# Kernel optimization log

Hardware: AMD Instinct MI355X
Metric: run time of the kernel (lower is better)

Reference implementation:

```python
import jax, jax.numpy as jnp
import numpy as np

B, S, D, H = 2, 4096, 512, 8
HD = D // H

def setup_inputs() -> dict:
    key = jax.random.key(0)
    ks = jax.random.split(key, 11)
    s = 1.0 / np.sqrt(D)
    return {
        "x": jax.random.normal(ks[0], (B, S, D), jnp.float32),
        "y": jax.random.normal(ks[1], (B, S, D), jnp.float32),
        "z": jax.random.normal(ks[2], (B, S, D), jnp.float32),
        "Wq": jax.random.normal(ks[3], (D, D), jnp.float32) * s,
        "bq": jnp.zeros((D,), jnp.float32),
        "Wk": jax.random.normal(ks[4], (D, D), jnp.float32) * s,
        "bk": jnp.zeros((D,), jnp.float32),
        "Wv": jax.random.normal(ks[5], (D, D), jnp.float32) * s,
        "bv": jnp.zeros((D,), jnp.float32),
        "Wp": jax.random.normal(ks[6], (D, D), jnp.float32) * s,
        "bp": jnp.zeros((D,), jnp.float32),
    }

def reference(x, y, z, Wq, bq, Wk, bk, Wv, bv, Wp, bp):
    # q/k/v projections, split heads: [B,S,D] -> [B,H,S,HD]
    def heads(t):
        return t.reshape(B, -1, H, HD).transpose(0, 2, 1, 3)
    q = heads(x @ Wq + bq)
    k = heads(y @ Wk + bk)
    v = heads(z @ Wv + bv)
    att = jnp.einsum('bhqd,bhkd->bhqk', q, k) / np.sqrt(HD).astype(np.float32)
    att = jax.nn.softmax(att, axis=-1)  # dropout is identity in eval mode
    out = jnp.einsum('bhqk,bhkd->bhqd', att, v)
    out = out.transpose(0, 2, 1, 3).reshape(B, -1, D)
    return out @ Wp + bp
```

## Files before the change

kernel.cpp:

```cpp
#include <hip/hip_runtime.h>
#include <math.h>

#define B_ 2
#define S_ 4096
#define D_ 512
#define H_ 8
#define HD_ 64
#define NROW_ (B_ * S_)
#define NELEM_ ((size_t)NROW_ * D_)
#define WELEM_ ((size_t)D_ * D_)
#define QSC 0.18033688f

typedef _Float16 half8 __attribute__((ext_vector_type(8)));
typedef _Float16 half4v __attribute__((ext_vector_type(4)));
typedef __fp16 fp16x2 __attribute__((ext_vector_type(2)));
typedef float floatx4 __attribute__((ext_vector_type(4)));

__device__ __forceinline__ half8 cvt_half8(float4 a, float4 b) {
  fp16x2 l0 = __builtin_amdgcn_cvt_pkrtz(a.x, a.y);
  fp16x2 l1 = __builtin_amdgcn_cvt_pkrtz(a.z, a.w);
  fp16x2 l2 = __builtin_amdgcn_cvt_pkrtz(b.x, b.y);
  fp16x2 l3 = __builtin_amdgcn_cvt_pkrtz(b.z, b.w);
  half8 h;
  h[0] = l0[0]; h[1] = l0[1]; h[2] = l1[0]; h[3] = l1[1];
  h[4] = l2[0]; h[5] = l2[1]; h[6] = l3[0]; h[7] = l3[1];
  return h;
}

__device__ __forceinline__ void async_lds16(const _Float16* g,
                                            _Float16* l) {
  __builtin_amdgcn_global_load_lds(
      (const __attribute__((address_space(1))) void*)g,
      (__attribute__((address_space(3))) void*)l, 16, 0, 0);
}

struct WPtrs { const float *W0, *W1, *W2, *W3; };

__global__ void wT4_kernel(WPtrs p, _Float16* __restrict__ WTbase) {
  __shared__ float tl[32][33];
  const int z = blockIdx.z;
  const float* W = z == 0 ? p.W0 : z == 1 ? p.W1 : z == 2 ? p.W2 : p.W3;
  const float scale = z == 0 ? QSC : 1.0f;
  _Float16* Wt = WTbase + (size_t)z * WELEM_;
  const int t = threadIdx.x;
  const int k0 = blockIdx.y * 32, n0 = blockIdx.x * 32;
  const int r = t >> 3, c0 = (t & 7) * 4;
  const float4 v = *(const float4*)&W[(size_t)(k0 + r) * D_ + n0 + c0];
  tl[r][c0 + 0] = v.x; tl[r][c0 + 1] = v.y;
  tl[r][c0 + 2] = v.z; tl[r][c0 + 3] = v.w;
  __syncthreads();
  half4v hv;
#pragma unroll
  for (int j = 0; j < 4; ++j) hv[j] = (_Float16)(tl[c0 + j][r] * scale);
  *(half4v*)&Wt[(size_t)(n0 + r) * D_ + k0 + c0] = hv;
}

__global__ void vT_kernel(const _Float16* __restrict__ Vh,
                          _Float16* __restrict__ VhT) {
  __shared__ alignas(16) _Float16 T[64][72];
  const int t = threadIdx.x;
  const int s0 = blockIdx.x * 64;
  const int h = blockIdx.y, b = blockIdx.z;
  const int srow = t >> 3, soff = (t & 7) * 8;
#pragma unroll
  for (int i = 0; i < 2; ++i)
    *(half8*)&T[srow + 32 * i][soff] = *(const half8*)
        &Vh[(size_t)(b * S_ + s0 + srow + 32 * i) * D_ + h * HD_ + soff];
  __syncthreads();
  const size_t obase = (size_t)(b * H_ + h) * HD_ * S_;
#pragma unroll
  for (int i = 0; i < 2; ++i) {
    half8 o;
#pragma unroll
    for (int j = 0; j < 8; ++j) o[j] = T[soff + j][srow + 32 * i];
    *(half8*)&VhT[obase + (size_t)(srow + 32 * i) * S_ + s0 + soff] = o;
  }
}

template <bool AF16, bool OUT16, int BM>
__device__ __forceinline__ void gemm_body(
    const void* __restrict__ Av, const _Float16* __restrict__ Bt,
    const float* __restrict__ bias, void* __restrict__ Cout, float bscale,
    int bx, int by, int tid) {
  constexpr int MT = BM / 32;
  __shared__ alignas(16) _Float16 As[BM][72];
  __shared__ alignas(16) _Float16 Bs[128][72];

  const int w = tid >> 6, lane = tid & 63;
  const int m = lane & 15, quad = lane >> 4;
  const int row0 = by * BM, col0 = bx * 128;
  const int wr = (w >> 1) * (BM / 2), wc = (w & 1) * 64;
  const int srow = tid >> 3, soff = (tid & 7) * 8;

  const _Float16* A16 = (const _Float16*)Av;
  const float* A32 = (const float*)Av;

  floatx4 acc[MT][4];
#pragma unroll
  for (int i = 0; i < MT; ++i)
#pragma unroll
    for (int j = 0; j < 4; ++j) acc[i][j] = floatx4{0.f, 0.f, 0.f, 0.f};

  half8 pa16[MT];
  float4 pa32[MT][2];
  half8 pb[4];
#pragma unroll
  for (int i = 0; i < MT; ++i) {
    const size_t ar = (size_t)(row0 + srow + 32 * i) * D_ + soff;
    if (AF16) pa16[i] = *(const half8*)&A16[ar];
    else { pa32[i][0] = *(const float4*)&A32[ar];
           pa32[i][1] = *(const float4*)&A32[ar + 4]; }
  }
#pragma unroll
  for (int i = 0; i < 4; ++i)
    pb[i] = *(const half8*)&Bt[(size_t)(col0 + srow + 32 * i) * D_ + soff];

  for (int kt = 0; kt < D_ / 64; ++kt) {
    if (kt) __syncthreads();
#pragma unroll
    for (int i = 0; i < MT; ++i)
      *(half8*)&As[srow + 32 * i][soff] =
          AF16 ? pa16[i] : cvt_half8(pa32[i][0], pa32[i][1]);
#pragma unroll
    for (int i = 0; i < 4; ++i) *(half8*)&Bs[srow + 32 * i][soff] = pb[i];
    __syncthreads();
    if (kt < D_ / 64 - 1) {
      const int kc = (kt + 1) * 64 + soff;
#pragma unroll
      for (int i = 0; i < MT; ++i) {
        const size_t ar = (size_t)(row0 + srow + 32 * i) * D_ + kc;
        if (AF16) pa16[i] = *(const half8*)&A16[ar];
        else { pa32[i][0] = *(const float4*)&A32[ar];
               pa32[i][1] = *(const float4*)&A32[ar + 4]; }
      }
#pragma unroll
      for (int i = 0; i < 4; ++i)
        pb[i] = *(const half8*)&Bt[(size_t)(col0 + srow + 32 * i) * D_ + kc];
    }
#pragma unroll
    for (int h = 0; h < 2; ++h) {
      half8 af[MT], bf[4];
#pragma unroll
      for (int mt = 0; mt < MT; ++mt)
        af[mt] = *(const half8*)&As[wr + mt * 16 + m][h * 32 + quad * 8];
#pragma unroll
      for (int nt = 0; nt < 4; ++nt)
        bf[nt] = *(const half8*)&Bs[wc + nt * 16 + m][h * 32 + quad * 8];
#pragma unroll
      for (int mt = 0; mt < MT; ++mt)
#pragma unroll
        for (int nt = 0; nt < 4; ++nt)
          acc[mt][nt] = __builtin_amdgcn_mfma_f32_16x16x32_f16(
              af[mt], bf[nt], acc[mt][nt], 0, 0, 0);
    }
  }

  float bv[4];
#pragma unroll
  for (int nt = 0; nt < 4; ++nt)
    bv[nt] = bias[col0 + wc + nt * 16 + m] * bscale;
#pragma unroll
  for (int mt = 0; mt < MT; ++mt)
#pragma unroll
    for (int nt = 0; nt < 4; ++nt)
#pragma unroll
      for (int r = 0; r < 4; ++r) {
        const int row = row0 + wr + mt * 16 + quad * 4 + r;
        const int col = col0 + wc + nt * 16 + m;
        const float vout = acc[mt][nt][r] + bv[nt];
        if (OUT16)
          ((_Float16*)Cout)[(size_t)row * D_ + col] = (_Float16)vout;
        else
          ((float*)Cout)[(size_t)row * D_ + col] = vout;
      }
}

struct QkvPtrs { const float *A0, *A1, *A2, *b0, *b1, *b2; };

__global__ __launch_bounds__(256, 3) void qkv_gemm_kernel(
    QkvPtrs p, const _Float16* __restrict__ WT, _Float16* __restrict__ Cb) {
  const int z = blockIdx.z;
  const float* A = z == 0 ? p.A0 : z == 1 ? p.A1 : p.A2;
  const float* bias = z == 0 ? p.b0 : z == 1 ? p.b1 : p.b2;
  gemm_body<false, true, 128>(A, WT + (size_t)z * WELEM_, bias,
                              Cb + (size_t)z * NELEM_, z == 0 ? QSC : 1.0f,
                              blockIdx.x, blockIdx.y, threadIdx.x);
}

__global__ __launch_bounds__(256, 2) void out_gemm_kernel(
    const _Float16* __restrict__ Oh, const _Float16* __restrict__ WpT,
    const float* __restrict__ bp, float* __restrict__ out) {
  gemm_body<true, false, 64>(Oh, WpT, bp, out, 1.0f, blockIdx.x, blockIdx.y,
                             threadIdx.x);
}

__global__ __launch_bounds__(256, 3) void attn_v4_kernel(
    const _Float16* __restrict__ Qg, const _Float16* __restrict__ Kg,
    const _Float16* __restrict__ VT, _Float16* __restrict__ Og) {
  __shared__ alignas(16) _Float16 smem[4][64 * 64];

  const int t = threadIdx.x;
  const int w = t >> 6, lane = t & 63;
  const int m = lane & 15, quad = lane >> 4;
  const int q0 = blockIdx.x * 64;
  const size_t base =
      (size_t)blockIdx.z * ((size_t)S_ * D_) + (size_t)blockIdx.y * HD_;
  const size_t vbase = (size_t)(blockIdx.z * H_ + blockIdx.y) * HD_ * S_;

  half8 qb[4][2];
#pragma unroll
  for (int nt = 0; nt < 4; ++nt)
#pragma unroll
    for (int hh = 0; hh < 2; ++hh)
      qb[nt][hh] = *(const half8*)
          &Qg[base + (size_t)(q0 + 16 * nt + m) * D_ + 32 * hh + 8 * quad];

  floatx4 oacc[4][4];
  float lpart[4];
#pragma unroll
  for (int i = 0; i < 4; ++i) {
    lpart[i] = 0.f;
#pragma unroll
    for (int j = 0; j < 4; ++j) oacc[i][j] = floatx4{0.f, 0.f, 0.f, 0.f};
  }
  const floatx4 z4 = floatx4{0.f, 0.f, 0.f, 0.f};

  const int sr = lane >> 3;
  const int sc = lane & 7;
  const int r0 = 16 * w + sr, r1 = r0 + 8;
  const _Float16* kg0 = Kg + base + (size_t)r0 * D_ + ((sc ^ (r0 & 7)) * 8);
  const _Float16* kg1 = Kg + base + (size_t)r1 * D_ + ((sc ^ (r1 & 7)) * 8);
  const _Float16* vg0 = VT + vbase + (size_t)r0 * S_ + ((sc ^ (r0 & 7)) * 8);
  const _Float16* vg1 = VT + vbase + (size_t)r1 * S_ + ((sc ^ (r1 & 7)) * 8);
  const size_t kstep = (size_t)64 * D_;
  const int ld0 = (16 * w) * 64, ld1 = ld0 + 512;

  async_lds16(kg0, &smem[0][ld0]);
  async_lds16(kg1, &smem[0][ld1]);
  async_lds16(vg0, &smem[2][ld0]);
  async_lds16(vg1, &smem[2][ld1]);
  kg0 += kstep; kg1 += kstep; vg0 += 64; vg1 += 64;
  __syncthreads();

  const int mx7 = m & 7;
  const int ka0_off = (16 * w + m) * 64 + ((quad ^ mx7) << 3);
  const int ka1_off = (16 * w + m) * 64 + (((4 + quad) ^ mx7) << 3);
  const int vck = 2 * w + (quad >> 1);
  const int va_off = (((vck ^ mx7) << 3) + 4 * (quad & 1)) + m * 64;

  for (int kt = 0; kt < S_ / 64; ++kt) {
    const int buf = kt & 1;
    const _Float16* kb = &smem[buf][0];
    const _Float16* vb = &smem[2 + buf][0];

    const half8 ka0 = *(const half8*)(kb + ka0_off);
    const half8 ka1 = *(const half8*)(kb + ka1_off);
    half4v va[4];
#pragma unroll
    for (int mt = 0; mt < 4; ++mt)
      va[mt] = *(const half4v*)(vb + va_off + mt * 16 * 64);

    if (kt < S_ / 64 - 1) {
      _Float16* kn = &smem[buf ^ 1][0];
      _Float16* vn = &smem[2 + (buf ^ 1)][0];
      async_lds16(kg0, kn + ld0);
      async_lds16(kg1, kn + ld1);
      async_lds16(vg0, vn + ld0);
      async_lds16(vg1, vn + ld1);
      kg0 += kstep; kg1 += kstep; vg0 += 64; vg1 += 64;
    }

    floatx4 sacc[4];
#pragma unroll
    for (int nt = 0; nt < 4; ++nt) {
      floatx4 s = __builtin_amdgcn_mfma_f32_16x16x32_f16(ka0, qb[nt][0], z4,
                                                         0, 0, 0);
      s = __builtin_amdgcn_mfma_f32_16x16x32_f16(ka1, qb[nt][1], s, 0, 0, 0);
      sacc[nt] = s;
    }

    half4v pbf[4];
#pragma unroll
    for (int nt = 0; nt < 4; ++nt) {
      const float p0 = exp2f(fminf(sacc[nt][0], 15.5f));
      const float p1 = exp2f(fminf(sacc[nt][1], 15.5f));
      const float p2 = exp2f(fminf(sacc[nt][2], 15.5f));
      const float p3 = exp2f(fminf(sacc[nt][3], 15.5f));
      lpart[nt] += (p0 + p1) + (p2 + p3);
      const fp16x2 lo = __builtin_amdgcn_cvt_pkrtz(p0, p1);
      const fp16x2 hi = __builtin_amdgcn_cvt_pkrtz(p2, p3);
      half4v pb;
      pb[0] = lo[0]; pb[1] = lo[1]; pb[2] = hi[0]; pb[3] = hi[1];
      pbf[nt] = pb;
    }

#pragma unroll
    for (int mt = 0; mt < 4; ++mt)
#pragma unroll
      for (int nt = 0; nt < 4; ++nt)
        oacc[mt][nt] = __builtin_amdgcn_mfma_f32_16x16x16f16(
            va[mt], pbf[nt], oacc[mt][nt], 0, 0, 0);

    __syncthreads();
  }

  float* ored = (float*)&smem[0][0];
  float* lred = ored + 64 * 67;

#pragma unroll
  for (int nt = 0; nt < 4; ++nt) {
    float v = lpart[nt];
    v += __shfl_xor(v, 16);
    v += __shfl_xor(v, 32);
    lpart[nt] = v;
  }
  if (quad == 0) {
#pragma unroll
    for (int nt = 0; nt < 4; ++nt) lred[w * 64 + 16 * nt + m] = lpart[nt];
  }

  for (int wv = 0; wv < 4; ++wv) {
    if (w == wv) {
#pragma unroll
      for (int mt = 0; mt < 4; ++mt)
#pragma unroll
        for (int nt = 0; nt < 4; ++nt)
#pragma unroll
          for (int r = 0; r < 4; ++r) {
            const int d = 16 * mt + 4 * quad + r;
            const int qq = 16 * nt + m;
            float v = oacc[mt][nt][r];
            if (wv) v += ored[d * 67 + qq];
            ored[d * 67 + qq] = v;
          }
    }
    __syncthreads();
  }

  const int qq = t >> 2, dg = (t & 3) * 16;
  const float li = 1.0f / (lred[qq] + lred[64 + qq] + lred[128 + qq] +
                           lred[192 + qq]);
  half8 o0, o1;
#pragma unroll
  for (int j = 0; j < 8; ++j) {
    o0[j] = (_Float16)(ored[(dg + j) * 67 + qq] * li);
    o1[j] = (_Float16)(ored[(dg + 8 + j) * 67 + qq] * li);
  }
  _Float16* op = Og + base + (size_t)(q0 + qq) * D_ + dg;
  *(half8*)op = o0;
  *(half8*)(op + 8) = o1;
}

extern "C" void kernel_launch(void* const* d_in, const int* in_sizes, int n_in,
                              void* d_out, int out_size, void* d_ws,
                              size_t ws_size, hipStream_t stream) {
  const float* x  = (const float*)d_in[0];
  const float* y  = (const float*)d_in[1];
  const float* z  = (const float*)d_in[2];
  const float* Wq = (const float*)d_in[3];
  const float* bq = (const float*)d_in[4];
  const float* Wk = (const float*)d_in[5];
  const float* bk = (const float*)d_in[6];
  const float* Wv = (const float*)d_in[7];
  const float* bv = (const float*)d_in[8];
  const float* Wp = (const float*)d_in[9];
  const float* bp = (const float*)d_in[10];

  _Float16* hws = (_Float16*)d_ws;
  _Float16* WT  = hws;
  _Float16* Qh  = WT + 4 * WELEM_;
  _Float16* Kh  = Qh + NELEM_;
  _Float16* Vh  = Kh + NELEM_;
  _Float16* Oh  = Vh + NELEM_;
  _Float16* VhT = Oh + NELEM_;

  WPtrs wp{Wq, Wk, Wv, Wp};
  wT4_kernel<<<dim3(16, 16, 4), 256, 0, stream>>>(wp, WT);

  QkvPtrs qp{x, y, z, bq, bk, bv};
  qkv_gemm_kernel<<<dim3(4, 64, 3), 256, 0, stream>>>(qp, WT, Qh);

  vT_kernel<<<dim3(S_ / 64, H_, B_), 256, 0, stream>>>(Vh, VhT);

  attn_v4_kernel<<<dim3(S_ / 64, H_, B_), 256, 0, stream>>>(Qh, Kh, VhT, Oh);

  out_gemm_kernel<<<dim3(4, 128), 256, 0, stream>>>(Oh, WT + 3 * WELEM_, bp,
                                                    (float*)d_out);
}
```

Baseline: 290.5 us.

## Software-pipeline QK^T MFMA of next tile with softmax and PV of current

Restructures the attention loop so the QK^T scores for the next key tile are computed while the exp2 and PV MFMAs of the current tile run. LDS reads for the next tile are issued right after a barrier at the top of each iteration, and V fragments are double-buffered in registers through a two-step unrolled lambda. It also drops the fminf clamp before exp2f. The clamp appears to guard against fp16 overflow with the fixed-max softmax, so removing it risks inf for large scores, and the extra live registers may reduce occupancy.

```diff
diff --git a/kernel.cpp b/kernel.cpp
--- a/kernel.cpp
+++ b/kernel.cpp
@@ -194,7 +194,7 @@
                              threadIdx.x);
 }
 
-__global__ __launch_bounds__(256, 3) void attn_v4_kernel(
+__global__ __launch_bounds__(256, 3) void attn_v5_kernel(
     const _Float16* __restrict__ Qg, const _Float16* __restrict__ Kg,
     const _Float16* __restrict__ VT, _Float16* __restrict__ Og) {
   __shared__ alignas(16) _Float16 smem[4][64 * 64];
@@ -235,6 +235,12 @@
   const size_t kstep = (size_t)64 * D_;
   const int ld0 = (16 * w) * 64, ld1 = ld0 + 512;
 
+  const int mx7 = m & 7;
+  const int ka0_off = (16 * w + m) * 64 + ((quad ^ mx7) << 3);
+  const int ka1_off = (16 * w + m) * 64 + (((4 + quad) ^ mx7) << 3);
+  const int vck = 2 * w + (quad >> 1);
+  const int va_off = (((vck ^ mx7) << 3) + 4 * (quad & 1)) + m * 64;
+
   async_lds16(kg0, &smem[0][ld0]);
   async_lds16(kg1, &smem[0][ld1]);
   async_lds16(vg0, &smem[2][ld0]);
@@ -242,50 +248,56 @@
   kg0 += kstep; kg1 += kstep; vg0 += 64; vg1 += 64;
   __syncthreads();
 
-  const int mx7 = m & 7;
-  const int ka0_off = (16 * w + m) * 64 + ((quad ^ mx7) << 3);
-  const int ka1_off = (16 * w + m) * 64 + (((4 + quad) ^ mx7) << 3);
-  const int vck = 2 * w + (quad >> 1);
-  const int va_off = (((vck ^ mx7) << 3) + 4 * (quad & 1)) + m * 64;
-
-  for (int kt = 0; kt < S_ / 64; ++kt) {
-    const int buf = kt & 1;
-    const _Float16* kb = &smem[buf][0];
-    const _Float16* vb = &smem[2 + buf][0];
-
-    const half8 ka0 = *(const half8*)(kb + ka0_off);
-    const half8 ka1 = *(const half8*)(kb + ka1_off);
-    half4v va[4];
-#pragma unroll
-    for (int mt = 0; mt < 4; ++mt)
-      va[mt] = *(const half4v*)(vb + va_off + mt * 16 * 64);
-
-    if (kt < S_ / 64 - 1) {
-      _Float16* kn = &smem[buf ^ 1][0];
-      _Float16* vn = &smem[2 + (buf ^ 1)][0];
-      async_lds16(kg0, kn + ld0);
-      async_lds16(kg1, kn + ld1);
-      async_lds16(vg0, vn + ld0);
-      async_lds16(vg1, vn + ld1);
-      kg0 += kstep; kg1 += kstep; vg0 += 64; vg1 += 64;
-    }
-
-    floatx4 sacc[4];
+  half8 ka0 = *(const half8*)(&smem[0][0] + ka0_off);
+  half8 ka1 = *(const half8*)(&smem[0][0] + ka1_off);
+  half4v va_a[4], va_b[4];
+#pragma unroll
+  for (int mt = 0; mt < 4; ++mt)
+    va_a[mt] = *(const half4v*)(&smem[2][0] + va_off + mt * 16 * 64);
+
+  async_lds16(kg0, &smem[1][ld0]);
+  async_lds16(kg1, &smem[1][ld1]);
+  async_lds16(vg0, &smem[3][ld0]);
+  async_lds16(vg1, &smem[3][ld1]);
+  kg0 += kstep; kg1 += kstep; vg0 += 64; vg1 += 64;
+
+  floatx4 sacc[4];
+#pragma unroll
+  for (int nt = 0; nt < 4; ++nt) {
+    floatx4 s = __builtin_amdgcn_mfma_f32_16x16x32_f16(ka0, qb[nt][0], z4,
+                                                       0, 0, 0);
+    sacc[nt] = __builtin_amdgcn_mfma_f32_16x16x32_f16(ka1, qb[nt][1], s,
+                                                      0, 0, 0);
+  }
+
+  auto body = [&](int kt, half4v* va_cur, half4v* va_nxt) {
+    const int nb = (kt + 1) & 1;
+    const bool haveNext = kt < S_ / 64 - 1;
+    if (haveNext) {
+      __syncthreads();
+      ka0 = *(const half8*)(&smem[nb][0] + ka0_off);
+      ka1 = *(const half8*)(&smem[nb][0] + ka1_off);
+#pragma unroll
+      for (int mt = 0; mt < 4; ++mt)
+        va_nxt[mt] = *(const half4v*)(&smem[2 + nb][0] + va_off + mt * 16 * 64);
+      if (kt < S_ / 64 - 2) {
+        _Float16* kn = &smem[nb ^ 1][0];
+        _Float16* vn = &smem[2 + (nb ^ 1)][0];
+        async_lds16(kg0, kn + ld0);
+        async_lds16(kg1, kn + ld1);
+        async_lds16(vg0, vn + ld0);
+        async_lds16(vg1, vn + ld1);
+        kg0 += kstep; kg1 += kstep; vg0 += 64; vg1 += 64;
+      }
+    }
+
+    half4v pbf[4];
 #pragma unroll
     for (int nt = 0; nt < 4; ++nt) {
-      floatx4 s = __builtin_amdgcn_mfma_f32_16x16x32_f16(ka0, qb[nt][0], z4,
-                                                         0, 0, 0);
-      s = __builtin_amdgcn_mfma_f32_16x16x32_f16(ka1, qb[nt][1], s, 0, 0, 0);
-      sacc[nt] = s;
-    }
-
-    half4v pbf[4];
-#pragma unroll
-    for (int nt = 0; nt < 4; ++nt) {
-      const float p0 = exp2f(fminf(sacc[nt][0], 15.5f));
-      const float p1 = exp2f(fminf(sacc[nt][1], 15.5f));
-      const float p2 = exp2f(fminf(sacc[nt][2], 15.5f));
-      const float p3 = exp2f(fminf(sacc[nt][3], 15.5f));
+      const float p0 = exp2f(sacc[nt][0]);
+      const float p1 = exp2f(sacc[nt][1]);
+      const float p2 = exp2f(sacc[nt][2]);
+      const float p3 = exp2f(sacc[nt][3]);
       lpart[nt] += (p0 + p1) + (p2 + p3);
       const fp16x2 lo = __builtin_amdgcn_cvt_pkrtz(p0, p1);
       const fp16x2 hi = __builtin_amdgcn_cvt_pkrtz(p2, p3);
@@ -294,15 +306,29 @@
       pbf[nt] = pb;
     }
 
+    if (haveNext) {
+#pragma unroll
+      for (int nt = 0; nt < 4; ++nt) {
+        floatx4 s = __builtin_amdgcn_mfma_f32_16x16x32_f16(ka0, qb[nt][0], z4,
+                                                           0, 0, 0);
+        sacc[nt] = __builtin_amdgcn_mfma_f32_16x16x32_f16(ka1, qb[nt][1], s,
+                                                          0, 0, 0);
+      }
+    }
+
 #pragma unroll
     for (int mt = 0; mt < 4; ++mt)
 #pragma unroll
       for (int nt = 0; nt < 4; ++nt)
         oacc[mt][nt] = __builtin_amdgcn_mfma_f32_16x16x16f16(
-            va[mt], pbf[nt], oacc[mt][nt], 0, 0, 0);
-
-    __syncthreads();
-  }
+            va_cur[mt], pbf[nt], oacc[mt][nt], 0, 0, 0);
+  };
+
+  for (int kt = 0; kt < S_ / 64; kt += 2) {
+    body(kt, va_a, va_b);
+    body(kt + 1, va_b, va_a);
+  }
+  __syncthreads();
 
   float* ored = (float*)&smem[0][0];
   float* lred = ored + 64 * 67;
@@ -382,7 +408,7 @@
 
   vT_kernel<<<dim3(S_ / 64, H_, B_), 256, 0, stream>>>(Vh, VhT);
 
-  attn_v4_kernel<<<dim3(S_ / 64, H_, B_), 256, 0, stream>>>(Qh, Kh, VhT, Oh);
+  attn_v5_kernel<<<dim3(S_ / 64, H_, B_), 256, 0, stream>>>(Qh, Kh, VhT, Oh);
 
   out_gemm_kernel<<<dim3(4, 128), 256, 0, stream>>>(Oh, WT + 3 * WELEM_, bp,
                                                     (float*)d_out);
```

After: 382.8 us. 1.32x slower.

## Software-pipeline attention loop so next QK^T MFMA overlaps current exp and PV

Applied to the files above, without the earlier changes.

Restructures the attention main loop into a two-phase unrolled pipeline. The S=QK^T MFMAs for tile kt+1 are issued while the exp/convert and PV MFMAs of tile kt run, with the LDS fragment loads and the barrier moved ahead. The goal is to hide the MFMA-to-exp dependency latency and cut stalls at the barrier. It also drops the fminf clamp before exp2f, which saves a few VALU ops but removes overflow protection, and it keeps extra sacc and V registers live.

```diff
diff --git a/kernel.cpp b/kernel.cpp
--- a/kernel.cpp
+++ b/kernel.cpp
@@ -194,7 +194,56 @@
                              threadIdx.x);
 }
 
-__global__ __launch_bounds__(256, 3) void attn_v4_kernel(
+#define ATTN_PHASE(KT, VACUR, VANXT)                                          \
+  {                                                                           \
+    const int kt_ = (KT);                                                     \
+    const int nb_ = (kt_ + 1) & 1;                                            \
+    const bool haveNext_ = kt_ < S_ / 64 - 1;                                 \
+    if (haveNext_) {                                                          \
+      __syncthreads();                                                        \
+      ka0 = *(const half8*)(&smem[nb_][0] + ka0_off);                         \
+      ka1 = *(const half8*)(&smem[nb_][0] + ka1_off);                         \
+      _Pragma("unroll") for (int mt = 0; mt < 4; ++mt)                        \
+          VANXT[mt] =                                                         \
+          *(const half4v*)(&smem[2 + nb_][0] + va_off + mt * 16 * 64);        \
+      if (kt_ < S_ / 64 - 2) {                                                \
+        _Float16* kn = &smem[nb_ ^ 1][0];                                     \
+        _Float16* vn = &smem[2 + (nb_ ^ 1)][0];                               \
+        async_lds16(kg0, kn + ld0);                                           \
+        async_lds16(kg1, kn + ld1);                                           \
+        async_lds16(vg0, vn + ld0);                                           \
+        async_lds16(vg1, vn + ld1);                                           \
+        kg0 += kstep; kg1 += kstep; vg0 += 64; vg1 += 64;                     \
+      }                                                                       \
+    }                                                                         \
+    half4v pbf[4];                                                            \
+    _Pragma("unroll") for (int nt = 0; nt < 4; ++nt) {                        \
+      const float p0 = exp2f(sacc[nt][0]);                                    \
+      const float p1 = exp2f(sacc[nt][1]);                                    \
+      const float p2 = exp2f(sacc[nt][2]);                                    \
+      const float p3 = exp2f(sacc[nt][3]);                                    \
+      lpart[nt] += (p0 + p1) + (p2 + p3);                                     \
+      const fp16x2 lo = __builtin_amdgcn_cvt_pkrtz(p0, p1);                   \
+      const fp16x2 hi = __builtin_amdgcn_cvt_pkrtz(p2, p3);                   \
+      half4v pb;                                                              \
+      pb[0] = lo[0]; pb[1] = lo[1]; pb[2] = hi[0]; pb[3] = hi[1];             \
+      pbf[nt] = pb;                                                           \
+    }                                                                         \
+    if (haveNext_) {                                                          \
+      _Pragma("unroll") for (int nt = 0; nt < 4; ++nt) {                      \
+        floatx4 s = __builtin_amdgcn_mfma_f32_16x16x32_f16(ka0, qb[nt][0],    \
+                                                           z4, 0, 0, 0);      \
+        sacc[nt] = __builtin_amdgcn_mfma_f32_16x16x32_f16(ka1, qb[nt][1], s,  \
+                                                          0, 0, 0);           \
+      }                                                                       \
+    }                                                                         \
+    _Pragma("unroll") for (int mt = 0; mt < 4; ++mt)                          \
+        _Pragma("unroll") for (int nt = 0; nt < 4; ++nt)                      \
+        oacc[mt][nt] = __builtin_amdgcn_mfma_f32_16x16x16f16(                 \
+            VACUR[mt], pbf[nt], oacc[mt][nt], 0, 0, 0);                       \
+  }
+
+__global__ __launch_bounds__(256, 3) void attn_v6_kernel(
     const _Float16* __restrict__ Qg, const _Float16* __restrict__ Kg,
     const _Float16* __restrict__ VT, _Float16* __restrict__ Og) {
   __shared__ alignas(16) _Float16 smem[4][64 * 64];
@@ -235,6 +284,12 @@
   const size_t kstep = (size_t)64 * D_;
   const int ld0 = (16 * w) * 64, ld1 = ld0 + 512;
 
+  const int mx7 = m & 7;
+  const int ka0_off = (16 * w + m) * 64 + ((quad ^ mx7) << 3);
+  const int ka1_off = (16 * w + m) * 64 + (((4 + quad) ^ mx7) << 3);
+  const int vck = 2 * w + (quad >> 1);
+  const int va_off = (((vck ^ mx7) << 3) + 4 * (quad & 1)) + m * 64;
+
   async_lds16(kg0, &smem[0][ld0]);
   async_lds16(kg1, &smem[0][ld1]);
   async_lds16(vg0, &smem[2][ld0]);
@@ -242,67 +297,33 @@
   kg0 += kstep; kg1 += kstep; vg0 += 64; vg1 += 64;
   __syncthreads();
 
-  const int mx7 = m & 7;
-  const int ka0_off = (16 * w + m) * 64 + ((quad ^ mx7) << 3);
-  const int ka1_off = (16 * w + m) * 64 + (((4 + quad) ^ mx7) << 3);
-  const int vck = 2 * w + (quad >> 1);
-  const int va_off = (((vck ^ mx7) << 3) + 4 * (quad & 1)) + m * 64;
-
-  for (int kt = 0; kt < S_ / 64; ++kt) {
-    const int buf = kt & 1;
-    const _Float16* kb = &smem[buf][0];
-    const _Float16* vb = &smem[2 + buf][0];
-
-    const half8 ka0 = *(const half8*)(kb + ka0_off);
-    const half8 ka1 = *(const half8*)(kb + ka1_off);
-    half4v va[4];
-#pragma unroll
-    for (int mt = 0; mt < 4; ++mt)
-      va[mt] = *(const half4v*)(vb + va_off + mt * 16 * 64);
-
-    if (kt < S_ / 64 - 1) {
-      _Float16* kn = &smem[buf ^ 1][0];
-      _Float16* vn = &smem[2 + (buf ^ 1)][0];
-      async_lds16(kg0, kn + ld0);
-      async_lds16(kg1, kn + ld1);
-      async_lds16(vg0, vn + ld0);
-      async_lds16(vg1, vn + ld1);
-      kg0 += kstep; kg1 += kstep; vg0 += 64; vg1 += 64;
-    }
-
-    floatx4 sacc[4];
-#pragma unroll
-    for (int nt = 0; nt < 4; ++nt) {
-      floatx4 s = __builtin_amdgcn_mfma_f32_16x16x32_f16(ka0, qb[nt][0], z4,
-                                                         0, 0, 0);
-      s = __builtin_amdgcn_mfma_f32_16x16x32_f16(ka1, qb[nt][1], s, 0, 0, 0);
-      sacc[nt] = s;
-    }
-
-    half4v pbf[4];
-#pragma unroll
-    for (int nt = 0; nt < 4; ++nt) {
-      const float p0 = exp2f(fminf(sacc[nt][0], 15.5f));
-      const float p1 = exp2f(fminf(sacc[nt][1], 15.5f));
-      const float p2 = exp2f(fminf(sacc[nt][2], 15.5f));
-      const float p3 = exp2f(fminf(sacc[nt][3], 15.5f));
-      lpart[nt] += (p0 + p1) + (p2 + p3);
-      const fp16x2 lo = __builtin_amdgcn_cvt_pkrtz(p0, p1);
-      const fp16x2 hi = __builtin_amdgcn_cvt_pkrtz(p2, p3);
-      half4v pb;
-      pb[0] = lo[0]; pb[1] = lo[1]; pb[2] = hi[0]; pb[3] = hi[1];
-      pbf[nt] = pb;
-    }
-
-#pragma unroll
-    for (int mt = 0; mt < 4; ++mt)
-#pragma unroll
-      for (int nt = 0; nt < 4; ++nt)
-        oacc[mt][nt] = __builtin_amdgcn_mfma_f32_16x16x16f16(
-            va[mt], pbf[nt], oacc[mt][nt], 0, 0, 0);
-
-    __syncthreads();
-  }
+  half8 ka0 = *(const half8*)(&smem[0][0] + ka0_off);
+  half8 ka1 = *(const half8*)(&smem[0][0] + ka1_off);
+  half4v va_a[4], va_b[4];
+#pragma unroll
+  for (int mt = 0; mt < 4; ++mt)
+    va_a[mt] = *(const half4v*)(&smem[2][0] + va_off + mt * 16 * 64);
+
+  async_lds16(kg0, &smem[1][ld0]);
+  async_lds16(kg1, &smem[1][ld1]);
+  async_lds16(vg0, &smem[3][ld0]);
+  async_lds16(vg1, &smem[3][ld1]);
+  kg0 += kstep; kg1 += kstep; vg0 += 64; vg1 += 64;
+
+  floatx4 sacc[4];
+#pragma unroll
+  for (int nt = 0; nt < 4; ++nt) {
+    floatx4 s = __builtin_amdgcn_mfma_f32_16x16x32_f16(ka0, qb[nt][0], z4,
+                                                       0, 0, 0);
+    sacc[nt] = __builtin_amdgcn_mfma_f32_16x16x32_f16(ka1, qb[nt][1], s,
+                                                      0, 0, 0);
+  }
+
+  for (int kt = 0; kt < S_ / 64; kt += 2) {
+    ATTN_PHASE(kt, va_a, va_b)
+    ATTN_PHASE(kt + 1, va_b, va_a)
+  }
+  __syncthreads();
 
   float* ored = (float*)&smem[0][0];
   float* lred = ored + 64 * 67;
@@ -382,7 +403,7 @@
 
   vT_kernel<<<dim3(S_ / 64, H_, B_), 256, 0, stream>>>(Vh, VhT);
 
-  attn_v4_kernel<<<dim3(S_ / 64, H_, B_), 256, 0, stream>>>(Qh, Kh, VhT, Oh);
+  attn_v6_kernel<<<dim3(S_ / 64, H_, B_), 256, 0, stream>>>(Qh, Kh, VhT, Oh);
 
   out_gemm_kernel<<<dim3(4, 128), 256, 0, stream>>>(Oh, WT + 3 * WELEM_, bp,
                                                     (float*)d_out);
```

Measured after the change: 409.8 us. 1.41x slower.
